# Kernel optimization log

Measured on AMD Instinct MI355X. Metric: run time of the kernel, lower is better.

The kernel has to match this reference:

```python
import jax, jax.numpy as jnp
import numpy as np

T, B, IN = 256, 64, 512
HIDDEN = [512, 512, 512]
DILATIONS = [1, 2, 4]


def _lstm_scan(x, W_ih, W_hh, b_ih, b_hh):
    """Run an LSTMCell over leading time axis of x: [Td, N, D] -> [Td, N, H]."""
    H = W_hh.shape[1]
    N = x.shape[1]
    h0 = jnp.zeros((N, H), x.dtype)
    c0 = jnp.zeros((N, H), x.dtype)

    def step(carry, xt):
        h, c = carry
        gates = xt @ W_ih.T + b_ih + h @ W_hh.T + b_hh  # [N, 4H], torch order i,f,g,o
        i, f, g, o = jnp.split(gates, 4, axis=-1)
        c = jax.nn.sigmoid(f) * c + jax.nn.sigmoid(i) * jnp.tanh(g)
        h = jax.nn.sigmoid(o) * jnp.tanh(c)
        return (h, c), h

    _, hs = jax.lax.scan(step, (h0, c0), x)
    return hs


def _drnn_layer(x, rate, W_ih, W_hh, b_ih, b_hh):
    """Dilated RNN layer. x: [T, B, D] with T % rate == 0.
    Torch code concats `rate` consecutive timesteps along batch -> one dilated step;
    reshape [T,B,D] -> [T//rate, rate*B, D] reproduces exactly that layout, and the
    chunk/unroll at the end is the inverse reshape."""
    Tn, Bn, D = x.shape
    Td = Tn // rate
    xd = x.reshape(Td, rate * Bn, D)
    hs = _lstm_scan(xd, W_ih, W_hh, b_ih, b_hh)  # [Td, rate*B, H]
    return hs.reshape(Tn, Bn, W_hh.shape[1])


def setup_inputs() -> dict:
    key = jax.random.key(0)
    ks = jax.random.split(key, 1 + 4 * len(HIDDEN))
    inp = {"x": jax.random.normal(ks[0], (T, B, IN), dtype=jnp.float32)}
    in_dim = IN
    ki = 1
    for li, H in enumerate(HIDDEN):
        bound = 1.0 / np.sqrt(H)
        inp[f"W_ih{li}"] = jax.random.uniform(ks[ki + 0], (4 * H, in_dim), jnp.float32, -bound, bound)
        inp[f"W_hh{li}"] = jax.random.uniform(ks[ki + 1], (4 * H, H), jnp.float32, -bound, bound)
        inp[f"b_ih{li}"] = jax.random.uniform(ks[ki + 2], (4 * H,), jnp.float32, -bound, bound)
        inp[f"b_hh{li}"] = jax.random.uniform(ks[ki + 3], (4 * H,), jnp.float32, -bound, bound)
        ki += 4
        in_dim = H
    return inp


def reference(x,
              W_ih0, W_hh0, b_ih0, b_hh0,
              W_ih1, W_hh1, b_ih1, b_hh1,
              W_ih2, W_hh2, b_ih2, b_hh2):
    params = [(W_ih0, W_hh0, b_ih0, b_hh0),
              (W_ih1, W_hh1, b_ih1, b_hh1),
              (W_ih2, W_hh2, b_ih2, b_hh2)]
    h = x
    for (Wih, Whh, bih, bhh), rate in zip(params, DILATIONS):
        h = _drnn_layer(h, rate, Wih, Whh, bih, bhh)
    return h  # [T, B, HIDDEN[-1]]
```

## Files before the change

### kernel.cpp

```cpp
#include <hip/hip_runtime.h>

typedef __attribute__((ext_vector_type(8))) short bf16x8;
typedef __attribute__((ext_vector_type(4))) float f32x4;

__device__ __forceinline__ unsigned short f2bf(float x) {
    unsigned u = __float_as_uint(x);
    u += 0x7FFFu + ((u >> 16) & 1u);
    return (unsigned short)(u >> 16);
}
__device__ __forceinline__ float sigm(float x) { return 1.0f / (1.0f + __expf(-x)); }
__device__ __forceinline__ float ftanh(float x) {
    float e = __expf(2.f * x);
    return 1.f - 2.f / (e + 1.f);
}

__device__ __forceinline__ void gld16(const unsigned short* g, unsigned short* l) {
    __builtin_amdgcn_global_load_lds((const __attribute__((address_space(1))) void*)g,
                                     (__attribute__((address_space(3))) void*)l, 16, 0, 0);
}

__device__ __forceinline__ void st_plain32(unsigned* p, unsigned v) {
    asm volatile("global_store_dword %0, %1, off" :: "v"(p), "v"(v) : "memory");
}
__device__ __forceinline__ void st_wt32(unsigned* p, unsigned v) {
    asm volatile("global_store_dword %0, %1, off sc0 sc1" :: "v"(p), "v"(v) : "memory");
}
__device__ __forceinline__ void aaddMALL(unsigned* p) {
    unsigned one = 1;
    asm volatile("global_atomic_add %0, %1, off sc1" :: "v"(p), "v"(one) : "memory");
}
__device__ __forceinline__ unsigned ld_mall(const unsigned* p) {
    unsigned v;
    asm volatile("global_load_dword %0, %1, off sc0 sc1\n\ts_waitcnt vmcnt(0)"
                 : "=v"(v) : "v"(p) : "memory");
    return v;
}
__device__ __forceinline__ void st_wt16(unsigned short* p, unsigned v) {
    asm volatile("global_store_short %0, %1, off sc0 sc1" :: "v"(p), "v"(v) : "memory");
}

__device__ __forceinline__ float dppx1(float x) {
    return __int_as_float(__builtin_amdgcn_mov_dpp(__float_as_int(x), 0xB1, 0xF, 0xF, true));
}
__device__ __forceinline__ float dppx2(float x) {
    return __int_as_float(__builtin_amdgcn_mov_dpp(__float_as_int(x), 0x4E, 0xF, 0xF, true));
}

__global__ __launch_bounds__(256) void k_conv_x(const float* __restrict__ x,
                                                unsigned short* __restrict__ Xp) {
    int i = blockIdx.x * 256 + threadIdx.x;
    int rb = i >> 10, kc = (i >> 6) & 15, ln = i & 63;
    int row = (rb << 4) + (ln & 15);
    int k   = (kc << 5) + ((ln >> 4) << 3);
    const float* s = x + (size_t)row * 512 + k;
    float4 v0 = *(const float4*)s, v1 = *(const float4*)(s + 4);
    unsigned short o[8] = {f2bf(v0.x), f2bf(v0.y), f2bf(v0.z), f2bf(v0.w),
                           f2bf(v1.x), f2bf(v1.y), f2bf(v1.z), f2bf(v1.w)};
    *(bf16x8*)(Xp + (size_t)i * 8) = *(bf16x8*)o;
}

__global__ __launch_bounds__(256) void k_conv_w(const float* __restrict__ Wih,
                                                const float* __restrict__ Whh,
                                                unsigned short* __restrict__ Wp) {
    int i = blockIdx.x * 256 + threadIdx.x;
    int wrb = i >> 11, kc = (i >> 6) & 31, ln = i & 63;
    int j = (wrb << 4) + (ln & 15);
    int k = (kc << 5) + ((ln >> 4) << 3);
    int srow = (j & 3) * 512 + (j >> 2);
    const float* s = (k < 512) ? (Wih + (size_t)srow * 512 + k)
                               : (Whh + (size_t)srow * 512 + (k - 512));
    float4 v0 = *(const float4*)s, v1 = *(const float4*)(s + 4);
    unsigned short o[8] = {f2bf(v0.x), f2bf(v0.y), f2bf(v0.z), f2bf(v0.w),
                           f2bf(v1.x), f2bf(v1.y), f2bf(v1.z), f2bf(v1.w)};
    *(bf16x8*)(Wp + (size_t)i * 8) = *(bf16x8*)o;
}

struct DP {
    const unsigned short* Xp;
    unsigned short *Hp0, *Hp1, *Hp2;
    unsigned short *Xq1, *Xq2;
    const unsigned short *Wp0, *Wp1, *Wp2;
    const float *bi0, *bh0, *bi1, *bh1, *bi2, *bh2;
    float* Out;
    unsigned int* flags;
};

__device__ __forceinline__ void quadT(f32x4 a, int sq, float& G0, float& G1, float& G2, float& G3) {
    float a0 = a[0], a1 = a[1], a2 = a[2], a3 = a[3];
    float p1 = (sq & 1) ? a0 : a1; float g1_ = dppx1(p1);
    float p2 = (sq & 1) ? a2 : a3; float g2_ = dppx1(p2);
    float m0 = (sq & 1) ? g1_ : a0, m1 = (sq & 1) ? a1 : g1_;
    float m2 = (sq & 1) ? g2_ : a2, m3 = (sq & 1) ? a3 : g2_;
    float q1 = (sq & 2) ? m0 : m2; float h1_ = dppx2(q1);
    float q2 = (sq & 2) ? m1 : m3; float h2_ = dppx2(q2);
    G0 = (sq & 2) ? h1_ : m0; G1 = (sq & 2) ? h2_ : m1;
    G2 = (sq & 2) ? m2 : h1_; G3 = (sq & 2) ? m3 : h2_;
}

#define PIN8(A,B,C,D,E,F,G,H) \
    asm volatile("" : "+v"(A),"+v"(B),"+v"(C),"+v"(D),"+v"(E),"+v"(F),"+v"(G),"+v"(H))
#define SBAR()  __builtin_amdgcn_sched_barrier(0)
#define MEMBAR() asm volatile("" ::: "memory")
#define RAWBAR() do { MEMBAR(); SBAR(); __builtin_amdgcn_s_barrier(); SBAR(); MEMBAR(); } while (0)
#define VMC(n) asm volatile("s_waitcnt vmcnt(" #n ")" ::: "memory")

__global__ __launch_bounds__(256, 1) void k_drnn(DP p) {
    const int tid = threadIdx.x, lane = tid & 63, wv = tid >> 6;
    const int l15 = lane & 15, lhi = lane >> 4, sq = l15 & 3;

    const int b = blockIdx.x;
    const int cid = b & 7, w = b >> 3;
    int l, c, T, P, N;
    if (cid < 2)      { l = 0; c = cid;     T = 256; P = 1; N = 64;  }
    else if (cid < 4) { l = 1; c = cid - 2; T = 128; P = 2; N = 128; }
    else              { l = 2; c = cid - 4; T = 64;  P = 2; N = 256; }

    const unsigned short* Xs = (l == 0) ? p.Xp  : (l == 1 ? p.Xq1 : p.Xq2);
    unsigned short*       Hd = (l == 0) ? p.Hp0 : (l == 1 ? p.Hp1 : p.Hp2);
    unsigned short*       Xw = (l == 0) ? p.Xq1 : (l == 1 ? p.Xq2 : nullptr);
    const unsigned short* Ws = (l == 0) ? p.Wp0 : (l == 1 ? p.Wp1 : p.Wp2);
    const float* bi = (l == 0) ? p.bi0 : (l == 1 ? p.bi1 : p.bi2);
    const float* bh = (l == 0) ? p.bh0 : (l == 1 ? p.bh1 : p.bh2);
    const int R0 = c * (P * 32);
    const int alias = (p.Xq1 == p.Hp0);

    __shared__ unsigned short At[65536];
    __shared__ unsigned pollbuf[32];

    const unsigned short* wbase = Ws + ((size_t)(((w << 2) + wv) * 32) << 9) + lane * 8;
#define DECLW(n) bf16x8 w##n = *(const bf16x8*)(wbase + (n << 9));
    DECLW(0) DECLW(1) DECLW(2) DECLW(3) DECLW(4) DECLW(5) DECLW(6) DECLW(7)
    DECLW(8) DECLW(9) DECLW(10) DECLW(11) DECLW(12) DECLW(13) DECLW(14) DECLW(15)
    DECLW(16) DECLW(17) DECLW(18) DECLW(19) DECLW(20) DECLW(21) DECLW(22) DECLW(23)
    DECLW(24) DECLW(25) DECLW(26) DECLW(27) DECLW(28) DECLW(29) DECLW(30) DECLW(31)

    const int hcol = (w << 4) + (wv << 2) + (l15 >> 2);
    const float bs0 = bi[hcol]        + bh[hcol];
    const float bs1 = bi[512 + hcol]  + bh[512 + hcol];
    const float bs2 = bi[1024 + hcol] + bh[1024 + hcol];
    const float bs3 = bi[1536 + hcol] + bh[1536 + hcol];

    const int kch = hcol >> 5;
    const int lane16 = (((hcol & 31) >> 3) << 4) + ((lhi << 2) + sq);
    const int st_lt = lane16 * 8 + (hcol & 7);

    float cst0 = 0.f, cst1 = 0.f, cst2 = 0.f, cst3 = 0.f;
    unsigned int* iflagV = p.flags;
    unsigned int* mflagV = p.flags + 256;
    unsigned int* cflagS = p.flags + 512;
    int fastok = 1;

#define KPX(na, nb, E0, E1, O0, O1, A0, A1) { \
    bf16x8 xa = *(const bf16x8*)((A0) + ((na) << 9)); \
    bf16x8 xb = *(const bf16x8*)((A1) + ((na) << 9)); \
    bf16x8 ya = *(const bf16x8*)((A0) + ((nb) << 9)); \
    bf16x8 yb = *(const bf16x8*)((A1) + ((nb) << 9)); \
    E0 = __builtin_amdgcn_mfma_f32_16x16x32_bf16(xa, w##na, E0, 0, 0, 0); \
    E1 = __builtin_amdgcn_mfma_f32_16x16x32_bf16(xb, w##na, E1, 0, 0, 0); \
    O0 = __builtin_amdgcn_mfma_f32_16x16x32_bf16(ya, w##nb, O0, 0, 0, 0); \
    O1 = __builtin_amdgcn_mfma_f32_16x16x32_bf16(yb, w##nb, O1, 0, 0, 0); }

#define XH(E0, E1, O0, O1, A0, A1) \
    KPX(0,1,E0,E1,O0,O1,A0,A1) KPX(2,3,E0,E1,O0,O1,A0,A1) \
    KPX(4,5,E0,E1,O0,O1,A0,A1) KPX(6,7,E0,E1,O0,O1,A0,A1) \
    KPX(8,9,E0,E1,O0,O1,A0,A1) KPX(10,11,E0,E1,O0,O1,A0,A1) \
    KPX(12,13,E0,E1,O0,O1,A0,A1) KPX(14,15,E0,E1,O0,O1,A0,A1)
#define HH(E0, E1, O0, O1, A0, A1) \
    KPX(16,17,E0,E1,O0,O1,A0,A1) KPX(18,19,E0,E1,O0,O1,A0,A1) \
    KPX(20,21,E0,E1,O0,O1,A0,A1) KPX(22,23,E0,E1,O0,O1,A0,A1) \
    KPX(24,25,E0,E1,O0,O1,A0,A1) KPX(26,27,E0,E1,O0,O1,A0,A1) \
    KPX(28,29,E0,E1,O0,O1,A0,A1) KPX(30,31,E0,E1,O0,O1,A0,A1)

#define PWC(RV, CSTV, HV) { \
    float G0, G1, G2, G3; quadT(RV, sq, G0, G1, G2, G3); \
    float cn = sigm(G1 + bs1) * CSTV + sigm(G0 + bs0) * ftanh(G2 + bs2); \
    HV = sigm(G3 + bs3) * ftanh(cn); CSTV = cn; }

#define STAGE_X(TT) { \
    const int RxN = ((TT) * N + R0) >> 4; \
    for (int i = 0; i < P * 8; ++i) { \
        int q = wv * (P * 8) + i, rb = q >> 4, kc = q & 15; \
        gld16(Xs + ((size_t)((RxN + rb) * 16 + kc) << 9) + lane * 8, \
              &At[(rb * 32 + kc) << 9]); } }
#define STAGE_H(TT) { \
    const int RhN = ((TT) * N + R0) >> 4; \
    for (int i = 0; i < P * 8; ++i) { \
        int q = wv * (P * 8) + i, rb = q >> 4, kc = q & 15; \
        gld16(Hd + ((size_t)((RhN + rb) * 16 + kc) << 9) + lane * 8, \
              &At[(rb * 32 + 16 + kc) << 9]); } }

#define CPOLL(TT) { \
    if (l == 1 && wv == 1 && lane < 2) { \
        const unsigned* cp = cflagS + lane * 32; \
        const unsigned need = 32u * (unsigned)(2 * (TT) + c + 1); \
        int n = 0; \
        while (!__all(ld_mall(cp) >= need)) { if (++n > (1 << 22)) break; } \
    } \
    if (l == 2 && wv == 1 && lane == 0) { \
        const unsigned* cp = cflagS + (2 + (c & 1)) * 32; \
        const unsigned need = 32u * (unsigned)(2 * (TT) + (c >> 1) + 1); \
        int n = 0; \
        while (ld_mall(cp) < need) { if (++n > (1 << 22)) break; } \
    } }

    f32x4 e0 = {0,0,0,0}, e1 = {0,0,0,0}, o0 = {0,0,0,0}, o1 = {0,0,0,0};
    f32x4 e2 = {0,0,0,0}, e3 = {0,0,0,0}, o2 = {0,0,0,0}, o3 = {0,0,0,0};
    const unsigned short* A00 = At + lane * 8;
    const unsigned short* A01 = A00 + (32 << 9);
    const unsigned short* A10 = A00 + (64 << 9);
    const unsigned short* A11 = A00 + (96 << 9);

    if (l > 0) CPOLL(0);
    RAWBAR();
    STAGE_X(0);
    VMC(0);
    RAWBAR();
    { XH(e0, e1, o0, o1, A00, A01) }
    if (P == 2) { XH(e2, e3, o2, o3, A10, A11) }

    for (int t = 0; t < T; ++t) {
        PIN8(w0,w1,w2,w3,w4,w5,w6,w7);
        PIN8(w8,w9,w10,w11,w12,w13,w14,w15);
        PIN8(w16,w17,w18,w19,w20,w21,w22,w23);
        PIN8(w24,w25,w26,w27,w28,w29,w30,w31);

        const int RxB = (t * N + R0) >> 4;

        if (t > 0) {
            if (wv == 0) {
                const unsigned need = (unsigned)t;
                const unsigned* mp = mflagV + cid * 32 + (lane & 31);
                if (t == T - 1 || !fastok) {
                    int n = 0;
                    while (!__all(ld_mall(mp) >= need)) { if (++n > (1 << 22)) break; }
                } else {
                    const unsigned short* gip = (const unsigned short*)(iflagV + cid * 32);
                    volatile unsigned* pb = pollbuf;
                    int n = 0;
                    for (;;) {
                        if (lane < 8) gld16(gip + lane * 8, (unsigned short*)pollbuf);
                        VMC(0);
                        SBAR();
                        unsigned v = pb[lane & 31];
                        if (__all((v - need) <= 1u)) break;
                        if (++n > 1024) {
                            fastok = 0;
                            int m = 0;
                            while (!__all(ld_mall(mp) >= need)) { if (++m > (1 << 22)) break; }
                            break;
                        }
                    }
                }
            }
            RAWBAR();
            STAGE_H(t - 1);
            VMC(0);
            RAWBAR();
            { HH(e0, e1, o0, o1, A00, A01) }
            if (P == 2) { HH(e2, e3, o2, o3, A10, A11) }
        }

        float hv0, hv1, hv2 = 0.f, hv3 = 0.f;
        { f32x4 r0 = e0 + o0, r1 = e1 + o1;
          PWC(r0, cst0, hv0) PWC(r1, cst1, hv1) }
        if (P == 2) {
          f32x4 r2 = e2 + o2, r3 = e3 + o3;
          PWC(r2, cst2, hv2) PWC(r3, cst3, hv3) }

        const unsigned short hb0 = f2bf(hv0), hb1 = f2bf(hv1);
        const unsigned short hb2 = f2bf(hv2), hb3 = f2bf(hv3);
        const size_t i0 = ((size_t)((RxB + 0) * 16 + kch) << 9) + st_lt;
        const size_t i1 = ((size_t)((RxB + 1) * 16 + kch) << 9) + st_lt;
        const size_t i2 = ((size_t)((RxB + 2) * 16 + kch) << 9) + st_lt;
        const size_t i3 = ((size_t)((RxB + 3) * 16 + kch) << 9) + st_lt;

        if (!alias || l == 2) {
            Hd[i0] = hb0; Hd[i1] = hb1;
            if (P == 2) { Hd[i2] = hb2; Hd[i3] = hb3; }
        }
        if (alias && l < 2) {
            st_wt16(Xw + i0, hb0); st_wt16(Xw + i1, hb1);
            if (P == 2) { st_wt16(Xw + i2, hb2); st_wt16(Xw + i3, hb3); }
        }
        if (l == 2) {
            p.Out[((size_t)(((RxB + 0) << 4) + (lhi << 2) + sq)) * 512 + hcol] = hv0;
            p.Out[((size_t)(((RxB + 1) << 4) + (lhi << 2) + sq)) * 512 + hcol] = hv1;
            p.Out[((size_t)(((RxB + 2) << 4) + (lhi << 2) + sq)) * 512 + hcol] = hv2;
            p.Out[((size_t)(((RxB + 3) << 4) + (lhi << 2) + sq)) * 512 + hcol] = hv3;
        }
        MEMBAR(); SBAR();

        if (t + 1 < T) {
            if (l == 0) {
                if (t == 0) RAWBAR();
                STAGE_X(t + 1);
                if (!alias) { st_wt16(Xw + i0, hb0); st_wt16(Xw + i1, hb1); }
                MEMBAR(); SBAR();
                if (!alias) VMC(10);
                else        VMC(8);
                RAWBAR();
                if (tid == 192) {
                    st_plain32(iflagV + cid * 32 + w, (unsigned)(t + 1));
                    st_wt32(mflagV + cid * 32 + w, (unsigned)(t + 1));
                    if (t > 0) aaddMALL(cflagS + cid * 32);
                }
                MEMBAR(); SBAR();
                if (!alias) {
                    if (wv == 3) { if (t > 0) VMC(5); else VMC(4); } else VMC(2);
                } else {
                    if (wv == 3) { if (t > 0) VMC(3); else VMC(2); } else VMC(0);
                }
            } else {
                CPOLL(t + 1);
                if (l == 2) VMC(4); else VMC(0);
                RAWBAR();
                STAGE_X(t + 1);
                if (l == 1 && !alias) {
                    st_wt16(Xw + i0, hb0); st_wt16(Xw + i1, hb1);
                    st_wt16(Xw + i2, hb2); st_wt16(Xw + i3, hb3);
                }
                MEMBAR(); SBAR();
                if (tid == 192) {
                    st_plain32(iflagV + cid * 32 + w, (unsigned)(t + 1));
                    st_wt32(mflagV + cid * 32 + w, (unsigned)(t + 1));
                    if (l == 1 && t > 0) aaddMALL(cflagS + cid * 32);
                }
                MEMBAR(); SBAR();
                if (l == 1) {
                    if (!alias) { if (wv == 3) { if (t > 0) VMC(7); else VMC(6); } else VMC(4); }
                    else        { if (wv == 3) { if (t > 0) VMC(3); else VMC(2); } else VMC(0); }
                } else {
                    if (wv == 3) VMC(2); else VMC(0);
                }
            }
            RAWBAR();
            e0 = (f32x4){0,0,0,0}; e1 = (f32x4){0,0,0,0};
            o0 = (f32x4){0,0,0,0}; o1 = (f32x4){0,0,0,0};
            { XH(e0, e1, o0, o1, A00, A01) }
            if (P == 2) {
                e2 = (f32x4){0,0,0,0}; e3 = (f32x4){0,0,0,0};
                o2 = (f32x4){0,0,0,0}; o3 = (f32x4){0,0,0,0};
                XH(e2, e3, o2, o3, A10, A11)
            }
        } else {
            if (!alias && l == 0) { st_wt16(Xw + i0, hb0); st_wt16(Xw + i1, hb1); }
            if (!alias && l == 1) { st_wt16(Xw + i0, hb0); st_wt16(Xw + i1, hb1);
                                    st_wt16(Xw + i2, hb2); st_wt16(Xw + i3, hb3); }
            MEMBAR(); SBAR();
            VMC(0);
            RAWBAR();
        }
    }

    VMC(0);
    __builtin_amdgcn_s_barrier();
    if (tid == 192) {
        st_plain32(iflagV + cid * 32 + w, (unsigned)T);
        st_wt32(mflagV + cid * 32 + w, (unsigned)T);
        if (l < 2) { aaddMALL(cflagS + cid * 32); aaddMALL(cflagS + cid * 32); }
    }
}

extern "C" void kernel_launch(void* const* d_in, const int* in_sizes, int n_in,
                              void* d_out, int out_size, void* d_ws, size_t ws_size,
                              hipStream_t stream)
{
    const float* x = (const float*)d_in[0];
    const float* Wih[3] = {(const float*)d_in[1], (const float*)d_in[5], (const float*)d_in[9]};
    const float* Whh[3] = {(const float*)d_in[2], (const float*)d_in[6], (const float*)d_in[10]};
    const float* bih[3] = {(const float*)d_in[3], (const float*)d_in[7], (const float*)d_in[11]};
    const float* bhh[3] = {(const float*)d_in[4], (const float*)d_in[8], (const float*)d_in[12]};

    char* wp = (char*)d_ws;
    const size_t SZ_A = (size_t)16384 * 512;
    unsigned int* flags = (unsigned int*)wp; wp += 4096;
    unsigned short* Xp  = (unsigned short*)wp; wp += SZ_A * 2;
    unsigned short* Hp0 = (unsigned short*)wp; wp += SZ_A * 2;
    unsigned short* Hp1 = (unsigned short*)wp; wp += SZ_A * 2;
    unsigned short* Hp2 = (unsigned short*)wp; wp += SZ_A * 2;
    unsigned short* Wp[3];
    for (int l = 0; l < 3; ++l) { Wp[l] = (unsigned short*)wp; wp += (size_t)2048 * 1024 * 2; }
    unsigned short* Xq1 = (unsigned short*)wp; wp += SZ_A * 2;
    unsigned short* Xq2 = (unsigned short*)wp; wp += SZ_A * 2;
    const size_t need = (size_t)(wp - (char*)d_ws);
    if (ws_size < need) { Xq1 = Hp0; Xq2 = Hp1; }

    hipMemsetAsync(flags, 0, 4096, stream);
    k_conv_x<<<dim3(4096), dim3(256), 0, stream>>>(x, Xp);
    for (int l = 0; l < 3; ++l)
        k_conv_w<<<dim3(1024), dim3(256), 0, stream>>>(Wih[l], Whh[l], Wp[l]);

    DP dp;
    dp.Xp = Xp; dp.Hp0 = Hp0; dp.Hp1 = Hp1; dp.Hp2 = Hp2;
    dp.Xq1 = Xq1; dp.Xq2 = Xq2;
    dp.Wp0 = Wp[0]; dp.Wp1 = Wp[1]; dp.Wp2 = Wp[2];
    dp.bi0 = bih[0]; dp.bh0 = bhh[0];
    dp.bi1 = bih[1]; dp.bh1 = bhh[1];
    dp.bi2 = bih[2]; dp.bh2 = bhh[2];
    dp.Out = (float*)d_out; dp.flags = flags;

    k_drnn<<<dim3(256), dim3(256), 0, stream>>>(dp);
}
```

Before: 883.0 us.

## Replace atomic counter flags with per-workgroup padded progress flags for cross-layer sync

Removes the MALL atomic-add counters that signalled cross-layer readiness and has consumer layers poll the producer layer's per-workgroup progress flags directly. All flags now sit 128 bytes apart, giving each its own cache line, and the fast-path poll fetches each flag separately. This avoids atomic contention and false sharing on flag lines, but each poll now issues 32 separate lines of loads instead of one contiguous load, and the flag region and memset grow to 64KB.

```diff
diff --git a/kernel.cpp b/kernel.cpp
--- a/kernel.cpp
+++ b/kernel.cpp
@@ -24,10 +24,6 @@
 }
 __device__ __forceinline__ void st_wt32(unsigned* p, unsigned v) {
     asm volatile("global_store_dword %0, %1, off sc0 sc1" :: "v"(p), "v"(v) : "memory");
-}
-__device__ __forceinline__ void aaddMALL(unsigned* p) {
-    unsigned one = 1;
-    asm volatile("global_atomic_add %0, %1, off sc1" :: "v"(p), "v"(one) : "memory");
 }
 __device__ __forceinline__ unsigned ld_mall(const unsigned* p) {
     unsigned v;
@@ -125,7 +121,7 @@
     const int alias = (p.Xq1 == p.Hp0);
 
     __shared__ unsigned short At[65536];
-    __shared__ unsigned pollbuf[32];
+    __shared__ unsigned pollbuf[128];
 
     const unsigned short* wbase = Ws + ((size_t)(((w << 2) + wv) * 32) << 9) + lane * 8;
 #define DECLW(n) bf16x8 w##n = *(const bf16x8*)(wbase + (n << 9));
@@ -145,9 +141,8 @@
     const int st_lt = lane16 * 8 + (hcol & 7);
 
     float cst0 = 0.f, cst1 = 0.f, cst2 = 0.f, cst3 = 0.f;
-    unsigned int* iflagV = p.flags;
-    unsigned int* mflagV = p.flags + 256;
-    unsigned int* cflagS = p.flags + 512;
+    unsigned int* iflagL = p.flags;
+    unsigned int* mflagL = p.flags + 8192;
     int fastok = 1;
 
 #define KPX(na, nb, E0, E1, O0, O1, A0, A1) { \
@@ -189,18 +184,18 @@
         gld16(Hd + ((size_t)((RhN + rb) * 16 + kc) << 9) + lane * 8, \
               &At[(rb * 32 + 16 + kc) << 9]); } }
 
-#define CPOLL(TT) { \
-    if (l == 1 && wv == 1 && lane < 2) { \
-        const unsigned* cp = cflagS + lane * 32; \
-        const unsigned need = 32u * (unsigned)(2 * (TT) + c + 1); \
+#define MPOLL(TT) { \
+    if (l == 1 && wv == 1) { \
+        const unsigned* mp = mflagL + ((((lane >> 5) << 5) + (lane & 31)) << 5); \
+        unsigned nd = (unsigned)(2 * (TT) + c + 2); if (nd > 256u) nd = 256u; \
         int n = 0; \
-        while (!__all(ld_mall(cp) >= need)) { if (++n > (1 << 22)) break; } \
+        while (!__all(ld_mall(mp) >= nd)) { if (++n > (1 << 22)) break; } \
     } \
-    if (l == 2 && wv == 1 && lane == 0) { \
-        const unsigned* cp = cflagS + (2 + (c & 1)) * 32; \
-        const unsigned need = 32u * (unsigned)(2 * (TT) + (c >> 1) + 1); \
+    if (l == 2 && wv == 1) { \
+        const unsigned* mp = mflagL + ((((2 + (c & 1)) << 5) + (lane & 31)) << 5); \
+        unsigned nd = (unsigned)(2 * (TT) + (c >> 1) + 2); if (nd > 128u) nd = 128u; \
         int n = 0; \
-        while (ld_mall(cp) < need) { if (++n > (1 << 22)) break; } \
+        while (!__all(ld_mall(mp) >= nd)) { if (++n > (1 << 22)) break; } \
     } }
 
     f32x4 e0 = {0,0,0,0}, e1 = {0,0,0,0}, o0 = {0,0,0,0}, o1 = {0,0,0,0};
@@ -210,7 +205,7 @@
     const unsigned short* A10 = A00 + (64 << 9);
     const unsigned short* A11 = A00 + (96 << 9);
 
-    if (l > 0) CPOLL(0);
+    MPOLL(0);
     RAWBAR();
     STAGE_X(0);
     VMC(0);
@@ -229,19 +224,20 @@
         if (t > 0) {
             if (wv == 0) {
                 const unsigned need = (unsigned)t;
-                const unsigned* mp = mflagV + cid * 32 + (lane & 31);
+                const unsigned* mp = mflagL + (((cid << 5) + (lane & 31)) << 5);
                 if (t == T - 1 || !fastok) {
                     int n = 0;
                     while (!__all(ld_mall(mp) >= need)) { if (++n > (1 << 22)) break; }
                 } else {
-                    const unsigned short* gip = (const unsigned short*)(iflagV + cid * 32);
+                    const unsigned short* gip =
+                        (const unsigned short*)(iflagL + (((cid << 5) + (lane & 31)) << 5));
                     volatile unsigned* pb = pollbuf;
                     int n = 0;
                     for (;;) {
-                        if (lane < 8) gld16(gip + lane * 8, (unsigned short*)pollbuf);
+                        if (lane < 32) gld16(gip, (unsigned short*)pollbuf);
                         VMC(0);
                         SBAR();
-                        unsigned v = pb[lane & 31];
+                        unsigned v = pb[(lane & 31) * 4];
                         if (__all((v - need) <= 1u)) break;
                         if (++n > 1024) {
                             fastok = 0;
@@ -300,19 +296,15 @@
                 else        VMC(8);
                 RAWBAR();
                 if (tid == 192) {
-                    st_plain32(iflagV + cid * 32 + w, (unsigned)(t + 1));
-                    st_wt32(mflagV + cid * 32 + w, (unsigned)(t + 1));
-                    if (t > 0) aaddMALL(cflagS + cid * 32);
+                    st_plain32(iflagL + (((cid << 5) + w) << 5), (unsigned)(t + 1));
+                    st_wt32(mflagL + (((cid << 5) + w) << 5), (unsigned)(t + 1));
                 }
                 MEMBAR(); SBAR();
-                if (!alias) {
-                    if (wv == 3) { if (t > 0) VMC(5); else VMC(4); } else VMC(2);
-                } else {
-                    if (wv == 3) { if (t > 0) VMC(3); else VMC(2); } else VMC(0);
-                }
+                if (!alias) { if (wv == 3) VMC(4); else VMC(2); }
+                else        { if (wv == 3) VMC(2); else VMC(0); }
             } else {
-                CPOLL(t + 1);
-                if (l == 2) VMC(4); else VMC(0);
+                MPOLL(t + 1);
+                VMC(0);
                 RAWBAR();
                 STAGE_X(t + 1);
                 if (l == 1 && !alias) {
@@ -321,17 +313,12 @@
                 }
                 MEMBAR(); SBAR();
                 if (tid == 192) {
-                    st_plain32(iflagV + cid * 32 + w, (unsigned)(t + 1));
-                    st_wt32(mflagV + cid * 32 + w, (unsigned)(t + 1));
-                    if (l == 1 && t > 0) aaddMALL(cflagS + cid * 32);
+                    st_plain32(iflagL + (((cid << 5) + w) << 5), (unsigned)(t + 1));
+                    st_wt32(mflagL + (((cid << 5) + w) << 5), (unsigned)(t + 1));
                 }
                 MEMBAR(); SBAR();
-                if (l == 1) {
-                    if (!alias) { if (wv == 3) { if (t > 0) VMC(7); else VMC(6); } else VMC(4); }
-                    else        { if (wv == 3) { if (t > 0) VMC(3); else VMC(2); } else VMC(0); }
-                } else {
-                    if (wv == 3) VMC(2); else VMC(0);
-                }
+                if (l == 1 && !alias) { if (wv == 3) VMC(6); else VMC(4); }
+                else                  { if (wv == 3) VMC(2); else VMC(0); }
             }
             RAWBAR();
             e0 = (f32x4){0,0,0,0}; e1 = (f32x4){0,0,0,0};
@@ -355,9 +342,8 @@
     VMC(0);
     __builtin_amdgcn_s_barrier();
     if (tid == 192) {
-        st_plain32(iflagV + cid * 32 + w, (unsigned)T);
-        st_wt32(mflagV + cid * 32 + w, (unsigned)T);
-        if (l < 2) { aaddMALL(cflagS + cid * 32); aaddMALL(cflagS + cid * 32); }
+        st_plain32(iflagL + (((cid << 5) + w) << 5), (unsigned)T);
+        st_wt32(mflagL + (((cid << 5) + w) << 5), (unsigned)T);
     }
 }
 
@@ -373,7 +359,7 @@
 
     char* wp = (char*)d_ws;
     const size_t SZ_A = (size_t)16384 * 512;
-    unsigned int* flags = (unsigned int*)wp; wp += 4096;
+    unsigned int* flags = (unsigned int*)wp; wp += 65536;
     unsigned short* Xp  = (unsigned short*)wp; wp += SZ_A * 2;
     unsigned short* Hp0 = (unsigned short*)wp; wp += SZ_A * 2;
     unsigned short* Hp1 = (unsigned short*)wp; wp += SZ_A * 2;
@@ -385,7 +371,7 @@
     const size_t need = (size_t)(wp - (char*)d_ws);
     if (ws_size < need) { Xq1 = Hp0; Xq2 = Hp1; }
 
-    hipMemsetAsync(flags, 0, 4096, stream);
+    hipMemsetAsync(flags, 0, 65536, stream);
     k_conv_x<<<dim3(4096), dim3(256), 0, stream>>>(x, Xp);
     for (int l = 0; l < 3; ++l)
         k_conv_w<<<dim3(1024), dim3(256), 0, stream>>>(Wih[l], Whh[l], Wp[l]);
```

Result: no change. 897.6 us (+1.7%).
